# Kernel optimization log

Hardware: AMD Instinct MI355X
Metric: run time of the kernel (lower is better)

The kernel has to match this reference:

```python
import jax, jax.numpy as jnp
import numpy as np

NUM_EXPERTS = 64
TOP_K = 2
CAPACITY_FACTOR = 1.25
D_MODEL = 2048
BATCH, SEQ = 4, 4096


def setup_inputs() -> dict:
    key = jax.random.key(0)
    kx, kw = jax.random.split(key)
    x = jax.random.normal(kx, (BATCH, SEQ, D_MODEL), dtype=jnp.float32)
    # router weight: Linear(input_dim, num_experts, bias=False), init std=0.001
    W = jax.random.normal(kw, (NUM_EXPERTS, D_MODEL), dtype=jnp.float32) * 0.001
    return {"x": x, "W": W}


def reference(x, W):
    B, S, D = x.shape
    N = B * S  # combined batch of tokens
    E = NUM_EXPERTS
    k = TOP_K
    capacity = int(CAPACITY_FACTOR * N * k / E)  # static Python int

    x_flat = x.reshape(N, D)
    router_logits = jnp.einsum('nd,ed->ne', x_flat, W)  # [N, E]
    routing_weights = jax.nn.softmax(router_logits, axis=-1)

    top_k_weights, top_k_indices = jax.lax.top_k(routing_weights, k)  # [N, k]
    top_k_weights = top_k_weights / (top_k_weights.sum(-1, keepdims=True) + 1e-8)

    expert_counts = jnp.zeros((E,), dtype=jnp.float32)
    dispatch_mask = jnp.zeros((N, E), dtype=jnp.float32)
    token_ids = jnp.arange(N)

    # Sequential over k (fixed, small): within a k-step the capacity check uses
    # counts from previous steps only, matching the torch scatter semantics.
    for k_idx in range(k):
        expert_idx = top_k_indices[:, k_idx]            # [N]
        under_cap = expert_counts[expert_idx] < capacity  # [N] bool
        expert_counts = expert_counts + jax.ops.segment_sum(
            under_cap.astype(jnp.float32), expert_idx, num_segments=E)
        # top-k experts are distinct per token, so add == set on zero-init slots
        dispatch_mask = dispatch_mask.at[token_ids, expert_idx].add(
            jnp.where(under_cap, top_k_weights[:, k_idx], 0.0))

    # Tokens that got dropped everywhere go to the least-loaded expert with w=1
    unrouted = dispatch_mask.sum(-1) == 0                     # [N]
    least_loaded = jnp.argmax(capacity - expert_counts)       # scalar
    dispatch_mask = jnp.where(
        unrouted[:, None] & (jnp.arange(E)[None, :] == least_loaded),
        1.0, dispatch_mask)

    normalized_dispatch_mask = dispatch_mask / (dispatch_mask.sum(-1, keepdims=True) + 1e-8)

    router_z_loss = jnp.mean(jnp.square(router_logits))
    counts = normalized_dispatch_mask.sum(0)                  # [E]
    target_count = float(N * k / E)
    load_balance_loss = jnp.mean(jnp.square(counts / float(N) - target_count / float(N)))
    router_loss = 0.001 * jax.lax.stop_gradient(router_z_loss) \
                + 0.001 * jax.lax.stop_gradient(load_balance_loss)

    return (jax.lax.stop_gradient(routing_weights), normalized_dispatch_mask, router_loss)
```

## Files before the change

kernel.cpp:

```cpp
#include <hip/hip_runtime.h>
#include <hip/hip_bf16.h>
#include <math.h>

#define N_TOK 16384
#define D_MODEL 2048
#define N_EXP 64
#define CAPACITY 640
#define KSPLIT 4
#define KSLICE (D_MODEL / KSPLIT)
#define BK 32
#define XP 36
#define NREP 8

__global__ __launch_bounds__(256, 4) void k1_gemm(
    const float* __restrict__ x, const float* __restrict__ W,
    float* __restrict__ part) {
  __shared__ float xs[64][XP];
  __shared__ float ws[BK][N_EXP];

  const int t = threadIdx.x;
  const int ks = blockIdx.x >> 8;
  const int grp = blockIdx.x & 255;
  const int m0 = grp * 64;
  const int kb = ks * KSLICE;

  const int tr = t >> 4;
  const int tc = t & 15;
  const int xr = t >> 2;
  const int xc = (t & 3) * 8;
  const int we = t & 63;
  const int wc = (t >> 6) * 8;

  const float* xg = x + (size_t)(m0 + xr) * D_MODEL + kb + xc;
  const float* wg = W + (size_t)we * D_MODEL + kb + wc;

  float4 xp0 = *(const float4*)xg, xp1 = *(const float4*)(xg + 4);
  float4 wp0 = *(const float4*)wg, wp1 = *(const float4*)(wg + 4);

  float acc[4][4] = {};

  for (int s = 0; s < KSLICE / BK; s++) {
    __syncthreads();
    *(float4*)&xs[xr][xc] = xp0;
    *(float4*)&xs[xr][xc + 4] = xp1;
    ws[wc + 0][we] = wp0.x; ws[wc + 1][we] = wp0.y;
    ws[wc + 2][we] = wp0.z; ws[wc + 3][we] = wp0.w;
    ws[wc + 4][we] = wp1.x; ws[wc + 5][we] = wp1.y;
    ws[wc + 6][we] = wp1.z; ws[wc + 7][we] = wp1.w;
    __syncthreads();
    if (s + 1 < KSLICE / BK) {
      const int d = (s + 1) * BK;
      xp0 = *(const float4*)(xg + d); xp1 = *(const float4*)(xg + d + 4);
      wp0 = *(const float4*)(wg + d); wp1 = *(const float4*)(wg + d + 4);
    }
#pragma unroll
    for (int k4 = 0; k4 < BK / 4; k4++) {
      float4 a[4], w4[4];
#pragma unroll
      for (int i = 0; i < 4; i++)
        a[i] = *(const float4*)&xs[tr + 16 * i][k4 * 4];
#pragma unroll
      for (int kk = 0; kk < 4; kk++)
        w4[kk] = *(const float4*)&ws[k4 * 4 + kk][tc * 4];
#pragma unroll
      for (int kk = 0; kk < 4; kk++)
#pragma unroll
        for (int i = 0; i < 4; i++) {
          const float av = (&a[i].x)[kk];
          acc[i][0] = fmaf(av, w4[kk].x, acc[i][0]);
          acc[i][1] = fmaf(av, w4[kk].y, acc[i][1]);
          acc[i][2] = fmaf(av, w4[kk].z, acc[i][2]);
          acc[i][3] = fmaf(av, w4[kk].w, acc[i][3]);
        }
    }
  }
#pragma unroll
  for (int i = 0; i < 4; i++) {
    float* pp = part + ((size_t)ks * N_TOK + m0 + tr + 16 * i) * N_EXP + tc * 4;
    *(float4*)pp = make_float4(acc[i][0], acc[i][1], acc[i][2], acc[i][3]);
  }
}

__global__ __launch_bounds__(256) void k2_softmax(
    const float* __restrict__ part, float* __restrict__ rw_out,
    int2* __restrict__ top12, float2* __restrict__ wts,
    int* __restrict__ histR, float* __restrict__ zR) {
  __shared__ float zred[4];
  const int lane = threadIdx.x & 63;
  const int wid = threadIdx.x >> 6;
  const int n = blockIdx.x * 4 + wid;
  const int rep = blockIdx.x & (NREP - 1);

  float v = 0.f;
#pragma unroll
  for (int s = 0; s < KSPLIT; s++)
    v += part[((size_t)s * N_TOK + n) * N_EXP + lane];

  float zp = v * v;
#pragma unroll
  for (int off = 32; off; off >>= 1) zp += __shfl_xor(zp, off);

  float m = v;
#pragma unroll
  for (int off = 32; off; off >>= 1) m = fmaxf(m, __shfl_xor(m, off));
  float p = __expf(v - m);
  float ssum = p;
#pragma unroll
  for (int off = 32; off; off >>= 1) ssum += __shfl_xor(ssum, off);
  const float rw = p / ssum;
  rw_out[(size_t)n * N_EXP + lane] = rw;

  const unsigned long long b1 = __ballot(v == m);
  const int i1 = __builtin_ctzll(b1);
  float v2 = (lane == i1) ? -INFINITY : v;
#pragma unroll
  for (int off = 32; off; off >>= 1) v2 = fmaxf(v2, __shfl_xor(v2, off));
  const unsigned long long b2 = __ballot(v == v2) & ~(1ull << i1);
  const int i2 = __builtin_ctzll(b2);

  const float rw1 = __shfl(rw, i1);
  const float rw2 = __shfl(rw, i2);
  if (lane == 0) {
    const float denom = rw1 + rw2 + 1e-8f;
    top12[n] = make_int2(i1, i2);
    wts[n] = make_float2(rw1 / denom, rw2 / denom);
    atomicAdd(&histR[(rep * N_EXP + i1) * 16], 1);
    zred[wid] = zp;
  }
  __syncthreads();
  if (threadIdx.x == 0)
    atomicAdd(&zR[rep * 16], zred[0] + zred[1] + zred[2] + zred[3]);
}

__global__ __launch_bounds__(256) void k3_dispatch(
    const int2* __restrict__ top12, const float2* __restrict__ wts,
    const int* __restrict__ histR, float* __restrict__ mask_out,
    float* __restrict__ cntR) {
  const int lane = threadIdx.x & 63;
  const int wid = threadIdx.x >> 6;
  const int n = blockIdx.x * 4 + wid;
  const int rep = blockIdx.x & (NREP - 1);

  const int2 ij = top12[n];
  const float2 w = wts[n];
  int h = 0;
#pragma unroll
  for (int r = 0; r < NREP; r++) h += histR[(r * N_EXP + ij.y) * 16];
  const bool allowed = h < CAPACITY;
  const float ssum = w.x + (allowed ? w.y : 0.f);
  const float inv = 1.f / (ssum + 1e-8f);
  float val = 0.f;
  if (lane == ij.x) val = w.x * inv;
  else if (allowed && lane == ij.y) val = w.y * inv;
  mask_out[(size_t)n * N_EXP + lane] = val;
  if (val != 0.f) atomicAdd(&cntR[(rep * N_EXP + lane) * 16], val);
}

__global__ void k4_loss(const float* __restrict__ cntR,
                        const float* __restrict__ zR,
                        float* __restrict__ loss_out) {
  const int lane = threadIdx.x;
  float c = 0.f;
#pragma unroll
  for (int r = 0; r < NREP; r++) c += cntR[(r * N_EXP + lane) * 16];
  const float d = (c - 512.0f) * (1.0f / 16384.0f);
  float v = d * d;
#pragma unroll
  for (int off = 32; off; off >>= 1) v += __shfl_xor(v, off);
  if (lane == 0) {
    float z = 0.f;
#pragma unroll
    for (int r = 0; r < NREP; r++) z += zR[r * 16];
    const float lb = v * (1.0f / 64.0f);
    loss_out[0] = 0.001f * (z * (1.0f / (16384.0f * 64.0f))) + 0.001f * lb;
  }
}

extern "C" void kernel_launch(void* const* d_in, const int* in_sizes, int n_in,
                              void* d_out, int out_size, void* d_ws, size_t ws_size,
                              hipStream_t stream) {
  const float* x = (const float*)d_in[0];
  const float* W = (const float*)d_in[1];
  float* out = (float*)d_out;
  float* rw_out = out;
  float* mask_out = out + (size_t)N_TOK * N_EXP;
  float* loss_out = out + 2 * (size_t)N_TOK * N_EXP;

  char* ws = (char*)d_ws;
  float* part = (float*)ws;
  int* histR = (int*)(ws + 16777216);
  float* cntR = (float*)(ws + 16777216 + 32768);
  float* zR = (float*)(ws + 16777216 + 65536);
  int2* top12 = (int2*)(ws + 16777216 + 131072);
  float2* wts = (float2*)(ws + 16777216 + 262144);

  hipMemsetAsync(histR, 0, 65536 + 512, stream);
  k1_gemm<<<KSPLIT * 256, 256, 0, stream>>>(x, W, part);
  k2_softmax<<<N_TOK / 4, 256, 0, stream>>>(part, rw_out, top12, wts, histR, zR);
  k3_dispatch<<<N_TOK / 4, 256, 0, stream>>>(top12, wts, histR, mask_out, cntR);
  k4_loss<<<1, 64, 0, stream>>>(cntR, zR, loss_out);
}
```

Baseline: 239.6 us.

## Fuse router GEMM with softmax using split-fp16 MFMA and drop split-K

```diff
diff --git a/kernel.cpp b/kernel.cpp
--- a/kernel.cpp
+++ b/kernel.cpp
@@ -1,135 +1,167 @@
 #include <hip/hip_runtime.h>
-#include <hip/hip_bf16.h>
 #include <math.h>
 
 #define N_TOK 16384
 #define D_MODEL 2048
 #define N_EXP 64
 #define CAPACITY 640
-#define KSPLIT 4
-#define KSLICE (D_MODEL / KSPLIT)
+#define NREP 8
+
 #define BK 32
-#define XP 36
-#define NREP 8
-
-__global__ __launch_bounds__(256, 4) void k1_gemm(
+#define NSTAGE (D_MODEL / BK)
+#define LP 48
+
+typedef __attribute__((ext_vector_type(8))) _Float16 h8;
+typedef __attribute__((ext_vector_type(4))) float f4;
+
+__global__ __launch_bounds__(256, 1) void k12_gemm_softmax(
     const float* __restrict__ x, const float* __restrict__ W,
-    float* __restrict__ part) {
-  __shared__ float xs[64][XP];
-  __shared__ float ws[BK][N_EXP];
+    float* __restrict__ rw_out, int2* __restrict__ top12,
+    float2* __restrict__ wts, int* __restrict__ histR,
+    float* __restrict__ zR) {
+  __shared__ _Float16 XH[2][64][LP];
+  __shared__ _Float16 XL[2][64][LP];
+  __shared__ _Float16 WHs[2][64][LP];
+  __shared__ _Float16 WLs[2][64][LP];
+  __shared__ float slog[64][65];
+  __shared__ float zred[4];
 
   const int t = threadIdx.x;
-  const int ks = blockIdx.x >> 8;
-  const int grp = blockIdx.x & 255;
-  const int m0 = grp * 64;
-  const int kb = ks * KSLICE;
-
-  const int tr = t >> 4;
-  const int tc = t & 15;
-  const int xr = t >> 2;
-  const int xc = (t & 3) * 8;
-  const int we = t & 63;
-  const int wc = (t >> 6) * 8;
-
-  const float* xg = x + (size_t)(m0 + xr) * D_MODEL + kb + xc;
-  const float* wg = W + (size_t)we * D_MODEL + kb + wc;
-
-  float4 xp0 = *(const float4*)xg, xp1 = *(const float4*)(xg + 4);
-  float4 wp0 = *(const float4*)wg, wp1 = *(const float4*)(wg + 4);
-
-  float acc[4][4] = {};
-
-  for (int s = 0; s < KSLICE / BK; s++) {
+  const int lane = t & 63;
+  const int wid = t >> 6;
+  const int m0 = blockIdx.x * 64;
+  const int rep = blockIdx.x & (NREP - 1);
+
+  const int srow = t >> 2;
+  const int scol = (t & 3) * 8;
+  const float* xg = x + (size_t)(m0 + srow) * D_MODEL + scol;
+  const float* wg = W + (size_t)srow * D_MODEL + scol;
+
+  float4 xa0 = *(const float4*)(xg);
+  float4 xa1 = *(const float4*)(xg + 4);
+  float4 wa0 = *(const float4*)(wg);
+  float4 wa1 = *(const float4*)(wg + 4);
+  float4 xb0 = *(const float4*)(xg + BK);
+  float4 xb1 = *(const float4*)(xg + BK + 4);
+  float4 wb0 = *(const float4*)(wg + BK);
+  float4 wb1 = *(const float4*)(wg + BK + 4);
+
+  f4 acc1[4], acc2[4];
+#pragma unroll
+  for (int i = 0; i < 4; i++) {
+    acc1[i] = (f4)(0.f);
+    acc2[i] = (f4)(0.f);
+  }
+
+#define CVT_STORE(buf, X0, X1, W0, W1)                              \
+  {                                                                 \
+    float xv[8] = {X0.x, X0.y, X0.z, X0.w, X1.x, X1.y, X1.z, X1.w}; \
+    float wv[8] = {W0.x, W0.y, W0.z, W0.w, W1.x, W1.y, W1.z, W1.w}; \
+    h8 cxh, cxl, cwh, cwl;                                          \
+    _Pragma("unroll") for (int j = 0; j < 8; j++) {                 \
+      _Float16 h = (_Float16)xv[j];                                 \
+      cxh[j] = h;                                                   \
+      cxl[j] = (_Float16)((xv[j] - (float)h) * 1024.f);             \
+      float wsc = wv[j] * 1024.f;                                   \
+      _Float16 hw = (_Float16)wsc;                                  \
+      cwh[j] = hw;                                                  \
+      cwl[j] = (_Float16)((wsc - (float)hw) * 1024.f);              \
+    }                                                               \
+    *(h8*)&XH[buf][srow][scol] = cxh;                               \
+    *(h8*)&XL[buf][srow][scol] = cxl;                               \
+    *(h8*)&WHs[buf][srow][scol] = cwh;                              \
+    *(h8*)&WLs[buf][srow][scol] = cwl;                              \
+  }
+
+#define COMPUTE(buf)                                                          \
+  {                                                                           \
+    const int frow = lane & 15;                                               \
+    const int fk = (lane >> 4) * 8;                                           \
+    h8 ah = *(const h8*)&XH[buf][wid * 16 + frow][fk];                        \
+    h8 al = *(const h8*)&XL[buf][wid * 16 + frow][fk];                        \
+    _Pragma("unroll") for (int nt = 0; nt < 4; nt++) {                        \
+      h8 bh = *(const h8*)&WHs[buf][nt * 16 + frow][fk];                      \
+      h8 bl = *(const h8*)&WLs[buf][nt * 16 + frow][fk];                      \
+      acc1[nt] =                                                              \
+          __builtin_amdgcn_mfma_f32_16x16x32_f16(ah, bh, acc1[nt], 0, 0, 0);  \
+      acc2[nt] =                                                              \
+          __builtin_amdgcn_mfma_f32_16x16x32_f16(al, bh, acc2[nt], 0, 0, 0);  \
+      acc2[nt] =                                                              \
+          __builtin_amdgcn_mfma_f32_16x16x32_f16(ah, bl, acc2[nt], 0, 0, 0);  \
+    }                                                                         \
+  }
+
+  CVT_STORE(0, xa0, xa1, wa0, wa1);
+  for (int it = 0; it < NSTAGE / 2; it++) {
     __syncthreads();
-    *(float4*)&xs[xr][xc] = xp0;
-    *(float4*)&xs[xr][xc + 4] = xp1;
-    ws[wc + 0][we] = wp0.x; ws[wc + 1][we] = wp0.y;
-    ws[wc + 2][we] = wp0.z; ws[wc + 3][we] = wp0.w;
-    ws[wc + 4][we] = wp1.x; ws[wc + 5][we] = wp1.y;
-    ws[wc + 6][we] = wp1.z; ws[wc + 7][we] = wp1.w;
+    const int s2 = 2 * it + 2;
+    if (s2 < NSTAGE) {
+      xa0 = *(const float4*)(xg + s2 * BK);
+      xa1 = *(const float4*)(xg + s2 * BK + 4);
+      wa0 = *(const float4*)(wg + s2 * BK);
+      wa1 = *(const float4*)(wg + s2 * BK + 4);
+    }
+    COMPUTE(0);
+    CVT_STORE(1, xb0, xb1, wb0, wb1);
     __syncthreads();
-    if (s + 1 < KSLICE / BK) {
-      const int d = (s + 1) * BK;
-      xp0 = *(const float4*)(xg + d); xp1 = *(const float4*)(xg + d + 4);
-      wp0 = *(const float4*)(wg + d); wp1 = *(const float4*)(wg + d + 4);
-    }
-#pragma unroll
-    for (int k4 = 0; k4 < BK / 4; k4++) {
-      float4 a[4], w4[4];
-#pragma unroll
-      for (int i = 0; i < 4; i++)
-        a[i] = *(const float4*)&xs[tr + 16 * i][k4 * 4];
-#pragma unroll
-      for (int kk = 0; kk < 4; kk++)
-        w4[kk] = *(const float4*)&ws[k4 * 4 + kk][tc * 4];
-#pragma unroll
-      for (int kk = 0; kk < 4; kk++)
-#pragma unroll
-        for (int i = 0; i < 4; i++) {
-          const float av = (&a[i].x)[kk];
-          acc[i][0] = fmaf(av, w4[kk].x, acc[i][0]);
-          acc[i][1] = fmaf(av, w4[kk].y, acc[i][1]);
-          acc[i][2] = fmaf(av, w4[kk].z, acc[i][2]);
-          acc[i][3] = fmaf(av, w4[kk].w, acc[i][3]);
-        }
-    }
-  }
-#pragma unroll
-  for (int i = 0; i < 4; i++) {
-    float* pp = part + ((size_t)ks * N_TOK + m0 + tr + 16 * i) * N_EXP + tc * 4;
-    *(float4*)pp = make_float4(acc[i][0], acc[i][1], acc[i][2], acc[i][3]);
-  }
-}
-
-__global__ __launch_bounds__(256) void k2_softmax(
-    const float* __restrict__ part, float* __restrict__ rw_out,
-    int2* __restrict__ top12, float2* __restrict__ wts,
-    int* __restrict__ histR, float* __restrict__ zR) {
-  __shared__ float zred[4];
-  const int lane = threadIdx.x & 63;
-  const int wid = threadIdx.x >> 6;
-  const int n = blockIdx.x * 4 + wid;
-  const int rep = blockIdx.x & (NREP - 1);
-
-  float v = 0.f;
-#pragma unroll
-  for (int s = 0; s < KSPLIT; s++)
-    v += part[((size_t)s * N_TOK + n) * N_EXP + lane];
-
-  float zp = v * v;
-#pragma unroll
-  for (int off = 32; off; off >>= 1) zp += __shfl_xor(zp, off);
-
-  float m = v;
-#pragma unroll
-  for (int off = 32; off; off >>= 1) m = fmaxf(m, __shfl_xor(m, off));
-  float p = __expf(v - m);
-  float ssum = p;
-#pragma unroll
-  for (int off = 32; off; off >>= 1) ssum += __shfl_xor(ssum, off);
-  const float rw = p / ssum;
-  rw_out[(size_t)n * N_EXP + lane] = rw;
-
-  const unsigned long long b1 = __ballot(v == m);
-  const int i1 = __builtin_ctzll(b1);
-  float v2 = (lane == i1) ? -INFINITY : v;
-#pragma unroll
-  for (int off = 32; off; off >>= 1) v2 = fmaxf(v2, __shfl_xor(v2, off));
-  const unsigned long long b2 = __ballot(v == v2) & ~(1ull << i1);
-  const int i2 = __builtin_ctzll(b2);
-
-  const float rw1 = __shfl(rw, i1);
-  const float rw2 = __shfl(rw, i2);
-  if (lane == 0) {
-    const float denom = rw1 + rw2 + 1e-8f;
-    top12[n] = make_int2(i1, i2);
-    wts[n] = make_float2(rw1 / denom, rw2 / denom);
-    atomicAdd(&histR[(rep * N_EXP + i1) * 16], 1);
-    zred[wid] = zp;
-  }
+    const int s3 = 2 * it + 3;
+    if (s3 < NSTAGE) {
+      xb0 = *(const float4*)(xg + s3 * BK);
+      xb1 = *(const float4*)(xg + s3 * BK + 4);
+      wb0 = *(const float4*)(wg + s3 * BK);
+      wb1 = *(const float4*)(wg + s3 * BK + 4);
+    }
+    COMPUTE(1);
+    if (it + 1 < NSTAGE / 2) CVT_STORE(0, xa0, xa1, wa0, wa1);
+  }
+
+  const int cg = lane >> 4, ci = lane & 15;
+#pragma unroll
+  for (int nt = 0; nt < 4; nt++)
+#pragma unroll
+    for (int r = 0; r < 4; r++) {
+      const float v =
+          (acc1[nt][r] + acc2[nt][r] * 0.0009765625f) * 0.0009765625f;
+      slog[wid * 16 + cg * 4 + r][nt * 16 + ci] = v;
+    }
+
+  float z_acc = 0.f;
+  for (int tt = 0; tt < 16; tt++) {
+    const int tloc = wid * 16 + tt;
+    const int n = m0 + tloc;
+    const float v = slog[tloc][lane];
+    z_acc += v * v;
+    float mx = v;
+#pragma unroll
+    for (int off = 32; off; off >>= 1) mx = fmaxf(mx, __shfl_xor(mx, off));
+    const float p = __expf(v - mx);
+    float ssum = p;
+#pragma unroll
+    for (int off = 32; off; off >>= 1) ssum += __shfl_xor(ssum, off);
+    const float rw = p / ssum;
+    rw_out[(size_t)n * N_EXP + lane] = rw;
+
+    const unsigned long long b1 = __ballot(v == mx);
+    const int i1 = __builtin_ctzll(b1);
+    float v2 = (lane == i1) ? -INFINITY : v;
+#pragma unroll
+    for (int off = 32; off; off >>= 1) v2 = fmaxf(v2, __shfl_xor(v2, off));
+    const unsigned long long b2 = __ballot(v == v2) & ~(1ull << i1);
+    const int i2 = __builtin_ctzll(b2);
+    const float rw1 = __shfl(rw, i1);
+    const float rw2 = __shfl(rw, i2);
+    if (lane == 0) {
+      const float denom = rw1 + rw2 + 1e-8f;
+      top12[n] = make_int2(i1, i2);
+      wts[n] = make_float2(rw1 / denom, rw2 / denom);
+      atomicAdd(&histR[(rep * N_EXP + i1) * 16], 1);
+    }
+  }
+#pragma unroll
+  for (int off = 32; off; off >>= 1) z_acc += __shfl_xor(z_acc, off);
+  if (lane == 0) zred[wid] = z_acc;
   __syncthreads();
-  if (threadIdx.x == 0)
-    atomicAdd(&zR[rep * 16], zred[0] + zred[1] + zred[2] + zred[3]);
+  if (t == 0) atomicAdd(&zR[rep * 16], zred[0] + zred[1] + zred[2] + zred[3]);
 }
 
 __global__ __launch_bounds__(256) void k3_dispatch(
@@ -177,8 +209,8 @@
 }
 
 extern "C" void kernel_launch(void* const* d_in, const int* in_sizes, int n_in,
-                              void* d_out, int out_size, void* d_ws, size_t ws_size,
-                              hipStream_t stream) {
+                              void* d_out, int out_size, void* d_ws,
+                              size_t ws_size, hipStream_t stream) {
   const float* x = (const float*)d_in[0];
   const float* W = (const float*)d_in[1];
   float* out = (float*)d_out;
@@ -187,16 +219,16 @@
   float* loss_out = out + 2 * (size_t)N_TOK * N_EXP;
 
   char* ws = (char*)d_ws;
-  float* part = (float*)ws;
-  int* histR = (int*)(ws + 16777216);
-  float* cntR = (float*)(ws + 16777216 + 32768);
-  float* zR = (float*)(ws + 16777216 + 65536);
-  int2* top12 = (int2*)(ws + 16777216 + 131072);
-  float2* wts = (float2*)(ws + 16777216 + 262144);
+  int* histR = (int*)ws;
+  float* cntR = (float*)(ws + 32768);
+  float* zR = (float*)(ws + 65536);
+  int2* top12 = (int2*)(ws + 131072);
+  float2* wts = (float2*)(ws + 262144);
 
   hipMemsetAsync(histR, 0, 65536 + 512, stream);
-  k1_gemm<<<KSPLIT * 256, 256, 0, stream>>>(x, W, part);
-  k2_softmax<<<N_TOK / 4, 256, 0, stream>>>(part, rw_out, top12, wts, histR, zR);
-  k3_dispatch<<<N_TOK / 4, 256, 0, stream>>>(top12, wts, histR, mask_out, cntR);
+  k12_gemm_softmax<<<256, 256, 0, stream>>>(x, W, rw_out, top12, wts, histR,
+                                            zR);
+  k3_dispatch<<<N_TOK / 4, 256, 0, stream>>>(top12, wts, histR, mask_out,
+                                             cntR);
   k4_loss<<<1, 64, 0, stream>>>(cntR, zR, loss_out);
 }
```

After: 223.7 us. 6.6% less time.
